# Kernel optimization log

Hardware: AMD Instinct MI355X
Metric: run time of the kernel (lower is better)

## Reference

```python
import jax, jax.numpy as jnp
import numpy as np

NUM_HEADS = 12  # head_dim = 768 // 12 = 64


def decomposed_rel_pos_bias(q, rel_pos_h, rel_pos_w, q_hw, k_hw):
    """Decomposed relative position bias (MViTv2 / SAM add_decomposed_rel_pos).
    q: (B*nH, q_h*q_w, head_dim). Returns bias (B*nH, q_h, q_w, k_h, k_w).
    q_size == k_size and rel_pos length == 2*size-1, so no interpolation branch.
    """
    q_h, q_w = q_hw
    k_h, k_w = k_hw
    # relative_coords = q_i - k_j + (k-1), values in [0, 2k-2]
    ch = jnp.arange(q_h)[:, None] - jnp.arange(k_h)[None, :] + (k_h - 1)
    cw = jnp.arange(q_w)[:, None] - jnp.arange(k_w)[None, :] + (k_w - 1)
    Rh = rel_pos_h[ch]  # (q_h, k_h, head_dim)
    Rw = rel_pos_w[cw]  # (q_w, k_w, head_dim)
    Bn, _, dim = q.shape
    r_q = q.reshape(Bn, q_h, q_w, dim)
    rel_h = jnp.einsum('bhwc,hkc->bhwk', r_q, Rh)  # (Bn, q_h, q_w, k_h)
    rel_w = jnp.einsum('bhwc,wkc->bhwk', r_q, Rw)  # (Bn, q_h, q_w, k_w)
    return rel_h[:, :, :, :, None] + rel_w[:, :, :, None, :]


def setup_inputs() -> dict:
    key = jax.random.key(0)
    ks = jax.random.split(key, 5)
    B, S, C = 200, 14, 768  # 200 windows of 14x14 tokens, dim 768
    hd = C // NUM_HEADS
    x = jax.random.normal(ks[0], (B, S, S, C), dtype=jnp.float32)
    w_qkv = jax.random.normal(ks[1], (C, 3 * C), dtype=jnp.float32) * (C ** -0.5)
    b_qkv = jnp.zeros((3 * C,), dtype=jnp.float32)
    w_proj = jax.random.normal(ks[2], (C, C), dtype=jnp.float32) * (C ** -0.5)
    b_proj = jnp.zeros((C,), dtype=jnp.float32)
    rel_pos_h = jax.random.normal(ks[3], (2 * S - 1, hd), dtype=jnp.float32) * 0.02
    rel_pos_w = jax.random.normal(ks[4], (2 * S - 1, hd), dtype=jnp.float32) * 0.02
    return {"x": x, "w_qkv": w_qkv, "b_qkv": b_qkv, "w_proj": w_proj,
            "b_proj": b_proj, "rel_pos_h": rel_pos_h, "rel_pos_w": rel_pos_w}


def reference(x, w_qkv, b_qkv, w_proj, b_proj, rel_pos_h, rel_pos_w):
    B, H, W, C = x.shape
    nH = NUM_HEADS
    hd = C // nH
    scale = hd ** -0.5
    # qkv projection: (B, H*W, 3*C)
    qkv = x.reshape(B, H * W, C) @ w_qkv + b_qkv
    qkv = qkv.reshape(B, H * W, 3, nH, hd).transpose(2, 0, 3, 1, 4)
    qkv = qkv.reshape(3, B * nH, H * W, hd)
    q, k, v = qkv[0], qkv[1], qkv[2]
    # attention scores with decomposed rel-pos bias
    attn = jnp.einsum('bqd,bkd->bqk', q * scale, k)  # (B*nH, HW, HW)
    bias = decomposed_rel_pos_bias(q, rel_pos_h, rel_pos_w, (H, W), (H, W))
    attn = attn.reshape(B * nH, H, W, H, W) + bias
    attn = jax.nn.softmax(attn.reshape(B * nH, H * W, H * W), axis=-1)
    out = jnp.einsum('bqk,bkd->bqd', attn, v)  # (B*nH, HW, hd)
    out = out.reshape(B, nH, H, W, hd).transpose(0, 2, 3, 1, 4).reshape(B, H, W, C)
    return out @ w_proj + b_proj
```

## Files before the change

kernel.cpp:

```cpp
#include <hip/hip_runtime.h>

typedef unsigned short u16;
typedef __attribute__((ext_vector_type(8))) __bf16 bf16x8;
typedef __attribute__((ext_vector_type(4))) float f32x4;
typedef __attribute__((ext_vector_type(4))) int i32x4;

#define MROWS 39200
#define MPAD  39296
#define KDIM  768

__device__ __forceinline__ u16 f2bf(float f) {
  unsigned u = __float_as_uint(f);
  return (u16)((u + 0x7fffu + ((u >> 16) & 1u)) >> 16);
}
__device__ __forceinline__ float bf2f(u16 b) {
  return __uint_as_float(((unsigned)b) << 16);
}
__device__ __forceinline__ f32x4 zero4() {
  f32x4 z; z[0] = 0.f; z[1] = 0.f; z[2] = 0.f; z[3] = 0.f; return z;
}
__device__ __forceinline__ void glds16(const void* g, void* l) {
  __builtin_amdgcn_global_load_lds((const __attribute__((address_space(1))) void*)(g),
                                   (__attribute__((address_space(3))) void*)(l), 16, 0, 0);
}

__global__ __launch_bounds__(256) void k_convert_x(const float* __restrict__ x,
                                                   u16* __restrict__ xb) {
  int idx = blockIdx.x * 256 + threadIdx.x;
  if (idx >= 3763200) return;
  f32x4 a = ((const f32x4*)x)[(size_t)idx * 2];
  f32x4 c = ((const f32x4*)x)[(size_t)idx * 2 + 1];
  u16 o[8];
  o[0] = f2bf(a[0]); o[1] = f2bf(a[1]); o[2] = f2bf(a[2]); o[3] = f2bf(a[3]);
  o[4] = f2bf(c[0]); o[5] = f2bf(c[1]); o[6] = f2bf(c[2]); o[7] = f2bf(c[3]);
  ((i32x4*)xb)[idx] = *(i32x4*)o;
}

__global__ __launch_bounds__(256) void k_transpose_w(const float* __restrict__ w,
                                                     u16* __restrict__ wT,
                                                     int K, int N, int total) {
  int idx = blockIdx.x * 256 + threadIdx.x;
  if (idx >= total) return;
  int n = idx / K, k = idx - n * K;
  wT[idx] = f2bf(w[(size_t)k * N + n]);
}

template <int MODE>
__global__ __launch_bounds__(256) void k_gemm(const u16* __restrict__ A,
                                              const u16* __restrict__ Bm,
                                              const float* __restrict__ bias,
                                              u16* __restrict__ o0,
                                              u16* __restrict__ o1,
                                              u16* __restrict__ o2,
                                              float* __restrict__ of) {
  __shared__ u16 a_sm[128 * 32];
  __shared__ u16 b_sm[128 * 32];
  const int tid = threadIdx.x, lane = tid & 63, wid = tid >> 6;
  const int tn = blockIdx.x, tm = blockIdx.y;
  const int lr = lane & 15, lg = lane >> 4;
  const int wm = wid >> 1, wn = wid & 1;

  const int o0b = wid * 2048 + lane * 16;
  const int o1b = o0b + 1024;
  const char* gA0 = (const char*)A + (size_t)(tm * 128 + (o0b >> 6)) * (KDIM * 2) + (o0b & 63);
  const char* gA1 = (const char*)A + (size_t)(tm * 128 + (o1b >> 6)) * (KDIM * 2) + (o1b & 63);
  const char* gB0 = (const char*)Bm + (size_t)(tn * 128 + (o0b >> 6)) * (KDIM * 2) + (o0b & 63);
  const char* gB1 = (const char*)Bm + (size_t)(tn * 128 + (o1b >> 6)) * (KDIM * 2) + (o1b & 63);
  char* lA0 = (char*)a_sm + wid * 2048;
  char* lA1 = lA0 + 1024;
  char* lB0 = (char*)b_sm + wid * 2048;
  char* lB1 = lB0 + 1024;

  f32x4 acc[4][4];
#pragma unroll
  for (int m = 0; m < 4; m++)
#pragma unroll
    for (int n = 0; n < 4; n++) acc[m][n] = zero4();

  for (int kt = 0; kt < KDIM / 32; kt++) {
    if (kt) __syncthreads();
    glds16(gA0 + kt * 64, lA0);
    glds16(gA1 + kt * 64, lA1);
    glds16(gB0 + kt * 64, lB0);
    glds16(gB1 + kt * 64, lB1);
    __syncthreads();
    bf16x8 af[4], bfr[4];
#pragma unroll
    for (int m = 0; m < 4; m++)
      af[m] = *(const bf16x8*)((const char*)a_sm + (wm * 64 + m * 16 + lr) * 64 + lg * 16);
#pragma unroll
    for (int n = 0; n < 4; n++)
      bfr[n] = *(const bf16x8*)((const char*)b_sm + (wn * 64 + n * 16 + lr) * 64 + lg * 16);
#pragma unroll
    for (int m = 0; m < 4; m++)
#pragma unroll
      for (int n = 0; n < 4; n++)
        acc[m][n] = __builtin_amdgcn_mfma_f32_16x16x32_bf16(af[m], bfr[n], acc[m][n], 0, 0, 0);
  }

#pragma unroll
  for (int n = 0; n < 4; n++) {
    int ng = tn * 128 + wn * 64 + n * 16 + lr;
    float bv = bias[ng];
#pragma unroll
    for (int m = 0; m < 4; m++) {
#pragma unroll
      for (int r = 0; r < 4; r++) {
        int mg = tm * 128 + wm * 64 + m * 16 + lg * 4 + r;
        if (mg < MROWS) {
          float val = acc[m][n][r] + bv;
          if (MODE == 0) {
            int which = ng / 768;
            int rem = ng - which * 768;
            int head = rem >> 6, d = rem & 63;
            int bi = mg / 196, i = mg - bi * 196;
            u16* dst = (which == 0) ? o0 : ((which == 1) ? o1 : o2);
            dst[((size_t)(bi * 12 + head) * 196 + i) * 64 + d] = f2bf(val);
          } else {
            of[(size_t)mg * 768 + ng] = val;
          }
        }
      }
    }
  }
}

#define SM_Q 0
#define SM_K 26624
#define SM_VT 53248
#define SM_P 81920
#define SM_RH 110592
#define SM_RW 122240
#define SM_TOTAL 133888

__global__ __launch_bounds__(256) void k_attn(const u16* __restrict__ qb,
                                              const u16* __restrict__ kb,
                                              const u16* __restrict__ vb,
                                              const float* __restrict__ rph,
                                              const float* __restrict__ rpw,
                                              u16* __restrict__ ao) {
  extern __shared__ char sm[];
  const int tid = threadIdx.x;
  const int bh = blockIdx.x;
  const size_t base = (size_t)bh * (196 * 64);

  for (int c = tid; c < 1568; c += 256) {
    int row = c >> 3, cb = (c & 7) << 4;
    int so = (row * 128 + cb) ^ ((row & 7) << 4);
    *(i32x4*)(sm + SM_Q + so) = *(const i32x4*)((const char*)(qb + base) + c * 16);
    *(i32x4*)(sm + SM_K + so) = *(const i32x4*)((const char*)(kb + base) + c * 16);
  }
  i32x4 zi; zi[0] = 0; zi[1] = 0; zi[2] = 0; zi[3] = 0;
  for (int c = tid; c < 96; c += 256) {
    int row = 196 + (c >> 3), cb = (c & 7) << 4;
    int so = (row * 128 + cb) ^ ((row & 7) << 4);
    *(i32x4*)(sm + SM_Q + so) = zi;
    *(i32x4*)(sm + SM_K + so) = zi;
  }
  for (int c = tid; c < 1568; c += 256) {
    int j = c >> 3, d0 = (c & 7) << 3;
    i32x4 vv = *(const i32x4*)((const char*)(vb + base) + c * 16);
    const u16* u = (const u16*)&vv;
#pragma unroll
    for (int e = 0; e < 8; e++) {
      int d = d0 + e;
      int so = (d * 448 + j * 2) ^ ((d & 7) << 4);
      *(u16*)(sm + SM_VT + so) = u[e];
    }
  }
  for (int idx = tid; idx < 64 * 28; idx += 256) {
    int d = idx / 28, j = 196 + (idx - d * 28);
    int so = (d * 448 + j * 2) ^ ((d & 7) << 4);
    *(u16*)(sm + SM_VT + so) = 0;
  }
  for (int idx = tid; idx < 1024; idx += 256) {
    int wv2 = idx >> 8, rem = idx & 255;
    int pr = rem >> 4, cc = 208 + (rem & 15);
    int so = wv2 * 7168 + ((pr * 448 + cc * 2) ^ ((pr & 7) << 4));
    *(u16*)(sm + SM_P + so) = 0;
  }
  __syncthreads();

  for (int e = tid; e < 208 * 14; e += 256) {
    int i = e / 14, kh = e - i * 14;
    float acc = 0.f;
    if (i < 196) {
      int h = i / 14;
      const float* R = rph + (h - kh + 13) * 64;
#pragma unroll
      for (int c8 = 0; c8 < 8; c8++) {
        int so = (i * 128 + c8 * 16) ^ ((i & 7) << 4);
        i32x4 v = *(const i32x4*)(sm + SM_Q + so);
        const u16* u = (const u16*)&v;
#pragma unroll
        for (int e2 = 0; e2 < 8; e2++) acc += bf2f(u[e2]) * R[c8 * 8 + e2];
      }
    }
    *(float*)(sm + SM_RH + e * 4) = acc;
  }
  for (int e = tid; e < 208 * 14; e += 256) {
    int i = e / 14, kw = e - i * 14;
    float acc = 0.f;
    if (i < 196) {
      int wq = i - (i / 14) * 14;
      const float* R = rpw + (wq - kw + 13) * 64;
#pragma unroll
      for (int c8 = 0; c8 < 8; c8++) {
        int so = (i * 128 + c8 * 16) ^ ((i & 7) << 4);
        i32x4 v = *(const i32x4*)(sm + SM_Q + so);
        const u16* u = (const u16*)&v;
#pragma unroll
        for (int e2 = 0; e2 < 8; e2++) acc += bf2f(u[e2]) * R[c8 * 8 + e2];
      }
    }
    *(float*)(sm + SM_RW + e * 4) = acc;
  }
  __syncthreads();

  const int lane = tid & 63, wv = tid >> 6;
  const int lr = lane & 15, lg = lane >> 4;
  const int bi = bh / 12, head = bh - bi * 12;

  for (int rt = wv; rt < 13; rt += 4) {
    int arow = rt * 16 + lr;
    bf16x8 aq0 = *(const bf16x8*)(sm + SM_Q + ((arow * 128 + lg * 16) ^ ((arow & 7) << 4)));
    bf16x8 aq1 = *(const bf16x8*)(sm + SM_Q + ((arow * 128 + 64 + lg * 16) ^ ((arow & 7) << 4)));
    f32x4 s[13];
#pragma unroll
    for (int j = 0; j < 13; j++) s[j] = zero4();
#pragma unroll
    for (int j = 0; j < 13; j++) {
      int brow = j * 16 + lr;
      bf16x8 bk0 = *(const bf16x8*)(sm + SM_K + ((brow * 128 + lg * 16) ^ ((brow & 7) << 4)));
      bf16x8 bk1 = *(const bf16x8*)(sm + SM_K + ((brow * 128 + 64 + lg * 16) ^ ((brow & 7) << 4)));
      s[j] = __builtin_amdgcn_mfma_f32_16x16x32_bf16(aq0, bk0, s[j], 0, 0, 0);
      s[j] = __builtin_amdgcn_mfma_f32_16x16x32_bf16(aq1, bk1, s[j], 0, 0, 0);
    }
    float rs[4];
#pragma unroll
    for (int r = 0; r < 4; r++) {
      int qi = rt * 16 + lg * 4 + r;
      float mx = -3.0e38f;
#pragma unroll
      for (int j = 0; j < 13; j++) {
        int col = j * 16 + lr;
        float t;
        if (col < 196) {
          int kh = (col * 2341) >> 15;
          int kw = col - kh * 14;
          t = s[j][r] * 0.125f + *(const float*)(sm + SM_RH + (qi * 14 + kh) * 4)
                               + *(const float*)(sm + SM_RW + (qi * 14 + kw) * 4);
        } else {
          t = -3.0e38f;
        }
        s[j][r] = t;
        mx = fmaxf(mx, t);
      }
      mx = fmaxf(mx, __shfl_xor(mx, 1));
      mx = fmaxf(mx, __shfl_xor(mx, 2));
      mx = fmaxf(mx, __shfl_xor(mx, 4));
      mx = fmaxf(mx, __shfl_xor(mx, 8));
      float sum = 0.f;
#pragma unroll
      for (int j = 0; j < 13; j++) {
        float p = __expf(s[j][r] - mx);
        s[j][r] = p;
        sum += p;
      }
      sum += __shfl_xor(sum, 1);
      sum += __shfl_xor(sum, 2);
      sum += __shfl_xor(sum, 4);
      sum += __shfl_xor(sum, 8);
      rs[r] = 1.f / sum;
    }
#pragma unroll
    for (int r = 0; r < 4; r++) {
      int pr = lg * 4 + r;
#pragma unroll
      for (int j = 0; j < 13; j++) {
        int col = j * 16 + lr;
        int so = wv * 7168 + ((pr * 448 + col * 2) ^ ((pr & 7) << 4));
        *(u16*)(sm + SM_P + so) = f2bf(s[j][r]);
      }
    }
    f32x4 ov[4];
#pragma unroll
    for (int d4 = 0; d4 < 4; d4++) ov[d4] = zero4();
#pragma unroll
    for (int kk = 0; kk < 7; kk++) {
      int soa = wv * 7168 + ((lr * 448 + kk * 64 + lg * 16) ^ ((lr & 7) << 4));
      bf16x8 pa = *(const bf16x8*)(sm + SM_P + soa);
#pragma unroll
      for (int d4 = 0; d4 < 4; d4++) {
        int vr = d4 * 16 + lr;
        int sob = (vr * 448 + kk * 64 + lg * 16) ^ ((vr & 7) << 4);
        bf16x8 vf = *(const bf16x8*)(sm + SM_VT + sob);
        ov[d4] = __builtin_amdgcn_mfma_f32_16x16x32_bf16(pa, vf, ov[d4], 0, 0, 0);
      }
    }
#pragma unroll
    for (int r = 0; r < 4; r++) {
      int i = rt * 16 + lg * 4 + r;
      if (i < 196) {
        size_t ro = ((size_t)(bi * 196 + i)) * 768 + head * 64;
#pragma unroll
        for (int d4 = 0; d4 < 4; d4++) {
          ao[ro + d4 * 16 + lr] = f2bf(ov[d4][r] * rs[r]);
        }
      }
    }
  }
}

extern "C" void kernel_launch(void* const* d_in, const int* in_sizes, int n_in,
                              void* d_out, int out_size, void* d_ws, size_t ws_size,
                              hipStream_t stream) {
  const float* x = (const float*)d_in[0];
  const float* w_qkv = (const float*)d_in[1];
  const float* b_qkv = (const float*)d_in[2];
  const float* w_proj = (const float*)d_in[3];
  const float* b_proj = (const float*)d_in[4];
  const float* rph = (const float*)d_in[5];
  const float* rpw = (const float*)d_in[6];
  float* out = (float*)d_out;

  char* ws = (char*)d_ws;
  u16* xb = (u16*)(ws + 0);
  u16* aob = (u16*)(ws + 0);
  u16* wqkvT = (u16*)(ws + 60358656);
  u16* wprojT = (u16*)(ws + 63897600);
  u16* qbuf = (u16*)(ws + 65077248);
  u16* kbuf = (u16*)(ws + 125288448);
  u16* vbuf = (u16*)(ws + 185499648);
  if (ws_size < 245710848ULL) return;

  k_convert_x<<<14700, 256, 0, stream>>>(x, xb);
  k_transpose_w<<<6912, 256, 0, stream>>>(w_qkv, wqkvT, 768, 2304, 768 * 2304);
  k_transpose_w<<<2304, 256, 0, stream>>>(w_proj, wprojT, 768, 768, 768 * 768);

  k_gemm<0><<<dim3(18, 307), 256, 0, stream>>>(xb, wqkvT, b_qkv, qbuf, kbuf, vbuf, nullptr);

  hipFuncSetAttribute((const void*)k_attn, hipFuncAttributeMaxDynamicSharedMemorySize, SM_TOTAL);
  k_attn<<<2400, 256, SM_TOTAL, stream>>>(qbuf, kbuf, vbuf, rph, rpw, aob);

  k_gemm<1><<<dim3(6, 307), 256, 0, stream>>>(aob, wprojT, b_proj, nullptr, nullptr, nullptr, out);
}
```

Baseline: 1.188 ms.

## Restructure attention kernel: MFMA rel-pos bias, register softmax, transposed V, XCD swizzle

Rewrites the attention kernel so the rel-pos bias projections run as MFMAs against a precomputed bf16 table instead of scalar loops. S is computed transposed so softmax reductions need only two cross-lane shuffles, and P is passed to the PV MFMA through register shuffles rather than an LDS round-trip. The QKV GEMM writes V pre-transposed, K is staged with global_load_lds, and LDS use drops to fit two blocks per CU. Both GEMMs gain an XCD-aware block remap for better L2 locality. Bias terms are now rounded to bf16, which adds some precision loss.

```diff
diff --git a/kernel.cpp b/kernel.cpp
--- a/kernel.cpp
+++ b/kernel.cpp
@@ -1,12 +1,13 @@
 #include <hip/hip_runtime.h>
 
 typedef unsigned short u16;
+typedef unsigned int u32;
 typedef __attribute__((ext_vector_type(8))) __bf16 bf16x8;
 typedef __attribute__((ext_vector_type(4))) float f32x4;
 typedef __attribute__((ext_vector_type(4))) int i32x4;
+typedef __attribute__((ext_vector_type(2))) int i32x2;
 
 #define MROWS 39200
-#define MPAD  39296
 #define KDIM  768
 
 __device__ __forceinline__ u16 f2bf(float f) {
@@ -22,6 +23,11 @@
 __device__ __forceinline__ void glds16(const void* g, void* l) {
   __builtin_amdgcn_global_load_lds((const __attribute__((address_space(1))) void*)(g),
                                    (__attribute__((address_space(3))) void*)(l), 16, 0, 0);
+}
+__device__ __forceinline__ u32 cvt_pk_bf16(float lo, float hi) {
+  u32 r;
+  asm volatile("v_cvt_pk_bf16_f32 %0, %1, %2" : "=v"(r) : "v"(lo), "v"(hi));
+  return r;
 }
 
 __global__ __launch_bounds__(256) void k_convert_x(const float* __restrict__ x,
@@ -45,6 +51,18 @@
   wT[idx] = f2bf(w[(size_t)k * N + n]);
 }
 
+__global__ __launch_bounds__(256) void k_prep_rpb(const float* __restrict__ rph,
+                                                  const float* __restrict__ rpw,
+                                                  u16* __restrict__ rpb) {
+  int idx = blockIdx.x * 256 + threadIdx.x;
+  if (idx >= 4096) return;
+  int p = idx >> 6, c = idx & 63;
+  float v = 0.f;
+  if (p < 27) v = rph[p * 64 + c];
+  else if (p >= 32 && p < 59) v = rpw[(p - 32) * 64 + c];
+  rpb[idx] = f2bf(v);
+}
+
 template <int MODE>
 __global__ __launch_bounds__(256) void k_gemm(const u16* __restrict__ A,
                                               const u16* __restrict__ Bm,
@@ -52,11 +70,15 @@
                                               u16* __restrict__ o0,
                                               u16* __restrict__ o1,
                                               u16* __restrict__ o2,
-                                              float* __restrict__ of) {
+                                              float* __restrict__ of,
+                                              int ntn, int swq, int swr) {
   __shared__ u16 a_sm[128 * 32];
   __shared__ u16 b_sm[128 * 32];
   const int tid = threadIdx.x, lane = tid & 63, wid = tid >> 6;
-  const int tn = blockIdx.x, tm = blockIdx.y;
+  int orig = blockIdx.x;
+  int xcd = orig & 7, jj = orig >> 3;
+  int wg = (xcd < swr ? xcd * (swq + 1) : swr * (swq + 1) + (xcd - swr) * swq) + jj;
+  const int tn = wg % ntn, tm = wg / ntn;
   const int lr = lane & 15, lg = lane >> 4;
   const int wm = wid >> 1, wn = wid & 1;
 
@@ -114,8 +136,13 @@
             int rem = ng - which * 768;
             int head = rem >> 6, d = rem & 63;
             int bi = mg / 196, i = mg - bi * 196;
-            u16* dst = (which == 0) ? o0 : ((which == 1) ? o1 : o2);
-            dst[((size_t)(bi * 12 + head) * 196 + i) * 64 + d] = f2bf(val);
+            int bh = bi * 12 + head;
+            if (which == 0)
+              o0[((size_t)bh * 196 + i) * 64 + d] = f2bf(val);
+            else if (which == 1)
+              o1[((size_t)bh * 196 + i) * 64 + d] = f2bf(val);
+            else
+              o2[((size_t)bh * 64 + d) * 196 + i] = f2bf(val);
           } else {
             of[(size_t)mg * 768 + ng] = val;
           }
@@ -125,187 +152,196 @@
   }
 }
 
-#define SM_Q 0
-#define SM_K 26624
-#define SM_VT 53248
-#define SM_P 81920
-#define SM_RH 110592
-#define SM_RW 122240
-#define SM_TOTAL 133888
-
-__global__ __launch_bounds__(256) void k_attn(const u16* __restrict__ qb,
-                                              const u16* __restrict__ kb,
-                                              const u16* __restrict__ vb,
-                                              const float* __restrict__ rph,
-                                              const float* __restrict__ rpw,
-                                              u16* __restrict__ ao) {
+#define AK 0
+#define AV 26624
+#define AT 55296
+#define SMT 78592
+
+__global__ __launch_bounds__(256, 2) void k_attn(const u16* __restrict__ qb,
+                                                 const u16* __restrict__ kb,
+                                                 const u16* __restrict__ vt,
+                                                 const u16* __restrict__ rpb,
+                                                 u16* __restrict__ ao) {
   extern __shared__ char sm[];
   const int tid = threadIdx.x;
   const int bh = blockIdx.x;
-  const size_t base = (size_t)bh * (196 * 64);
-
-  for (int c = tid; c < 1568; c += 256) {
-    int row = c >> 3, cb = (c & 7) << 4;
-    int so = (row * 128 + cb) ^ ((row & 7) << 4);
-    *(i32x4*)(sm + SM_Q + so) = *(const i32x4*)((const char*)(qb + base) + c * 16);
-    *(i32x4*)(sm + SM_K + so) = *(const i32x4*)((const char*)(kb + base) + c * 16);
-  }
-  i32x4 zi; zi[0] = 0; zi[1] = 0; zi[2] = 0; zi[3] = 0;
-  for (int c = tid; c < 96; c += 256) {
-    int row = 196 + (c >> 3), cb = (c & 7) << 4;
-    int so = (row * 128 + cb) ^ ((row & 7) << 4);
-    *(i32x4*)(sm + SM_Q + so) = zi;
-    *(i32x4*)(sm + SM_K + so) = zi;
-  }
-  for (int c = tid; c < 1568; c += 256) {
-    int j = c >> 3, d0 = (c & 7) << 3;
-    i32x4 vv = *(const i32x4*)((const char*)(vb + base) + c * 16);
-    const u16* u = (const u16*)&vv;
-#pragma unroll
-    for (int e = 0; e < 8; e++) {
-      int d = d0 + e;
-      int so = (d * 448 + j * 2) ^ ((d & 7) << 4);
-      *(u16*)(sm + SM_VT + so) = u[e];
-    }
-  }
-  for (int idx = tid; idx < 64 * 28; idx += 256) {
-    int d = idx / 28, j = 196 + (idx - d * 28);
-    int so = (d * 448 + j * 2) ^ ((d & 7) << 4);
-    *(u16*)(sm + SM_VT + so) = 0;
-  }
-  for (int idx = tid; idx < 1024; idx += 256) {
-    int wv2 = idx >> 8, rem = idx & 255;
-    int pr = rem >> 4, cc = 208 + (rem & 15);
-    int so = wv2 * 7168 + ((pr * 448 + cc * 2) ^ ((pr & 7) << 4));
-    *(u16*)(sm + SM_P + so) = 0;
-  }
-  __syncthreads();
-
-  for (int e = tid; e < 208 * 14; e += 256) {
-    int i = e / 14, kh = e - i * 14;
-    float acc = 0.f;
-    if (i < 196) {
-      int h = i / 14;
-      const float* R = rph + (h - kh + 13) * 64;
-#pragma unroll
-      for (int c8 = 0; c8 < 8; c8++) {
-        int so = (i * 128 + c8 * 16) ^ ((i & 7) << 4);
-        i32x4 v = *(const i32x4*)(sm + SM_Q + so);
-        const u16* u = (const u16*)&v;
-#pragma unroll
-        for (int e2 = 0; e2 < 8; e2++) acc += bf2f(u[e2]) * R[c8 * 8 + e2];
-      }
-    }
-    *(float*)(sm + SM_RH + e * 4) = acc;
-  }
-  for (int e = tid; e < 208 * 14; e += 256) {
-    int i = e / 14, kw = e - i * 14;
-    float acc = 0.f;
-    if (i < 196) {
-      int wq = i - (i / 14) * 14;
-      const float* R = rpw + (wq - kw + 13) * 64;
-#pragma unroll
-      for (int c8 = 0; c8 < 8; c8++) {
-        int so = (i * 128 + c8 * 16) ^ ((i & 7) << 4);
-        i32x4 v = *(const i32x4*)(sm + SM_Q + so);
-        const u16* u = (const u16*)&v;
-#pragma unroll
-        for (int e2 = 0; e2 < 8; e2++) acc += bf2f(u[e2]) * R[c8 * 8 + e2];
-      }
-    }
-    *(float*)(sm + SM_RW + e * 4) = acc;
-  }
-  __syncthreads();
-
   const int lane = tid & 63, wv = tid >> 6;
   const int lr = lane & 15, lg = lane >> 4;
+  const u16* qg = qb + (size_t)bh * 12544;
+  const u16* kg = kb + (size_t)bh * 12544;
+  const u16* vg = vt + (size_t)bh * 12544;
+
+  for (int o = tid * 16; o < 25088; o += 4096) {
+    int row = o >> 7, cb = o & 127;
+    glds16((const char*)kg + row * 128 + (cb ^ ((row & 7) << 4)), sm + AK + o);
+  }
+  for (int ch = tid; ch < 1600; ch += 256) {
+    int d = ch / 25, i = ch - d * 25;
+    const char* src = (const char*)vg + d * 392 + i * 16;
+    int dst = (d * 448 + i * 16) ^ ((d & 7) << 4);
+    if (i < 24) {
+      i32x2 va = *(const i32x2*)src;
+      i32x2 vb = *(const i32x2*)(src + 8);
+      *(i32x2*)(sm + AV + dst) = va;
+      *(i32x2*)(sm + AV + dst + 8) = vb;
+    } else {
+      i32x2 va = *(const i32x2*)src;
+      *(i32x2*)(sm + AV + dst) = va;
+    }
+  }
+  {
+    int d = tid >> 2, part = tid & 3;
+    if (part == 0) {
+      i32x2 z; z[0] = 0; z[1] = 0;
+      *(i32x2*)(sm + AV + ((d * 448 + 392) ^ ((d & 7) << 4))) = z;
+    } else {
+      i32x4 z; z[0] = 0; z[1] = 0; z[2] = 0; z[3] = 0;
+      *(i32x4*)(sm + AV + ((d * 448 + 384 + part * 16) ^ ((d & 7) << 4))) = z;
+    }
+  }
+  __syncthreads();
+
+  bf16x8 rb0[4], rb1[4];
+#pragma unroll
+  for (int pt = 0; pt < 4; pt++) {
+    rb0[pt] = *(const bf16x8*)((const char*)rpb + (pt * 16 + lr) * 128 + lg * 16);
+    rb1[pt] = *(const bf16x8*)((const char*)rpb + (pt * 16 + lr) * 128 + 64 + lg * 16);
+  }
+
   const int bi = bh / 12, head = bh - bi * 12;
 
-  for (int rt = wv; rt < 13; rt += 4) {
-    int arow = rt * 16 + lr;
-    bf16x8 aq0 = *(const bf16x8*)(sm + SM_Q + ((arow * 128 + lg * 16) ^ ((arow & 7) << 4)));
-    bf16x8 aq1 = *(const bf16x8*)(sm + SM_Q + ((arow * 128 + 64 + lg * 16) ^ ((arow & 7) << 4)));
+  for (int qt = wv; qt < 13; qt += 4) {
+    const int q = qt * 16 + lr;
+    const int qc = q > 195 ? 195 : q;
+    bf16x8 bq0 = *(const bf16x8*)((const char*)qg + qc * 128 + lg * 16);
+    bf16x8 bq1 = *(const bf16x8*)((const char*)qg + qc * 128 + 64 + lg * 16);
+
+    {
+      f32x4 td[4];
+#pragma unroll
+      for (int pt = 0; pt < 4; pt++) {
+        td[pt] = zero4();
+        td[pt] = __builtin_amdgcn_mfma_f32_16x16x32_bf16(bq0, rb0[pt], td[pt], 0, 0, 0);
+        td[pt] = __builtin_amdgcn_mfma_f32_16x16x32_bf16(bq1, rb1[pt], td[pt], 0, 0, 0);
+      }
+#pragma unroll
+      for (int pt = 0; pt < 4; pt++) {
+        int p = pt * 16 + lr;
+        int col = (p < 28) ? p : ((p >= 32 && p < 60) ? p - 4 : -1);
+        if (col >= 0) {
+#pragma unroll
+          for (int r = 0; r < 4; r++) {
+            int rowq = qt * 16 + lg * 4 + r;
+            *(u16*)(sm + AT + rowq * 112 + col * 2) = f2bf(td[pt][r]);
+          }
+        }
+      }
+      asm volatile("s_waitcnt lgkmcnt(0)" ::: "memory");
+    }
+
     f32x4 s[13];
 #pragma unroll
     for (int j = 0; j < 13; j++) s[j] = zero4();
 #pragma unroll
     for (int j = 0; j < 13; j++) {
-      int brow = j * 16 + lr;
-      bf16x8 bk0 = *(const bf16x8*)(sm + SM_K + ((brow * 128 + lg * 16) ^ ((brow & 7) << 4)));
-      bf16x8 bk1 = *(const bf16x8*)(sm + SM_K + ((brow * 128 + 64 + lg * 16) ^ ((brow & 7) << 4)));
-      s[j] = __builtin_amdgcn_mfma_f32_16x16x32_bf16(aq0, bk0, s[j], 0, 0, 0);
-      s[j] = __builtin_amdgcn_mfma_f32_16x16x32_bf16(aq1, bk1, s[j], 0, 0, 0);
-    }
-    float rs[4];
-#pragma unroll
-    for (int r = 0; r < 4; r++) {
-      int qi = rt * 16 + lg * 4 + r;
-      float mx = -3.0e38f;
-#pragma unroll
-      for (int j = 0; j < 13; j++) {
-        int col = j * 16 + lr;
-        float t;
-        if (col < 196) {
-          int kh = (col * 2341) >> 15;
-          int kw = col - kh * 14;
-          t = s[j][r] * 0.125f + *(const float*)(sm + SM_RH + (qi * 14 + kh) * 4)
-                               + *(const float*)(sm + SM_RW + (qi * 14 + kw) * 4);
-        } else {
-          t = -3.0e38f;
+      int kr = j * 16 + lr;
+      bf16x8 ak0 = *(const bf16x8*)(sm + AK + ((kr * 128 + lg * 16) ^ ((kr & 7) << 4)));
+      bf16x8 ak1 = *(const bf16x8*)(sm + AK + ((kr * 128 + 64 + lg * 16) ^ ((kr & 7) << 4)));
+      s[j] = __builtin_amdgcn_mfma_f32_16x16x32_bf16(ak0, bq0, s[j], 0, 0, 0);
+      s[j] = __builtin_amdgcn_mfma_f32_16x16x32_bf16(ak1, bq1, s[j], 0, 0, 0);
+    }
+
+    const int hq = (q * 2341) >> 15;
+    const int wq = q - hq * 14;
+    const char* Trow = sm + AT + q * 112;
+    float mx = -3.0e38f;
+#pragma unroll
+    for (int j = 0; j < 13; j++) {
+#pragma unroll
+      for (int r = 0; r < 4; r++) {
+        int k = j * 16 + lg * 4 + r;
+        float t = -3.0e38f;
+        if (k < 196) {
+          int kh = (k * 2341) >> 15;
+          int kw = k - kh * 14;
+          t = s[j][r] * 0.125f
+            + bf2f(*(const u16*)(Trow + (hq - kh + 13) * 2))
+            + bf2f(*(const u16*)(Trow + (wq - kw + 13 + 28) * 2));
         }
         s[j][r] = t;
         mx = fmaxf(mx, t);
       }
-      mx = fmaxf(mx, __shfl_xor(mx, 1));
-      mx = fmaxf(mx, __shfl_xor(mx, 2));
-      mx = fmaxf(mx, __shfl_xor(mx, 4));
-      mx = fmaxf(mx, __shfl_xor(mx, 8));
-      float sum = 0.f;
-#pragma unroll
-      for (int j = 0; j < 13; j++) {
-        float p = __expf(s[j][r] - mx);
+    }
+    mx = fmaxf(mx, __shfl_xor(mx, 16));
+    mx = fmaxf(mx, __shfl_xor(mx, 32));
+    float sum = 0.f;
+#pragma unroll
+    for (int j = 0; j < 13; j++) {
+#pragma unroll
+      for (int r = 0; r < 4; r++) {
+        int k = j * 16 + lg * 4 + r;
+        float p = 0.f;
+        if (k < 196) p = __expf(s[j][r] - mx);
         s[j][r] = p;
         sum += p;
       }
-      sum += __shfl_xor(sum, 1);
-      sum += __shfl_xor(sum, 2);
-      sum += __shfl_xor(sum, 4);
-      sum += __shfl_xor(sum, 8);
-      rs[r] = 1.f / sum;
-    }
-#pragma unroll
-    for (int r = 0; r < 4; r++) {
-      int pr = lg * 4 + r;
-#pragma unroll
-      for (int j = 0; j < 13; j++) {
-        int col = j * 16 + lr;
-        int so = wv * 7168 + ((pr * 448 + col * 2) ^ ((pr & 7) << 4));
-        *(u16*)(sm + SM_P + so) = f2bf(s[j][r]);
-      }
-    }
+    }
+    sum += __shfl_xor(sum, 16);
+    sum += __shfl_xor(sum, 32);
+    const float rs = 1.f / sum;
+
+    u32 w[13][2];
+#pragma unroll
+    for (int j = 0; j < 13; j++) {
+      w[j][0] = cvt_pk_bf16(s[j][0] * rs, s[j][1] * rs);
+      w[j][1] = cvt_pk_bf16(s[j][2] * rs, s[j][3] * rs);
+    }
+
+    const int srcA = lr + ((lg & 1) * 2) * 16;
+    const int srcB = srcA + 16;
+    const bool hi = (lg >> 1) != 0;
+
     f32x4 ov[4];
 #pragma unroll
     for (int d4 = 0; d4 < 4; d4++) ov[d4] = zero4();
+
 #pragma unroll
     for (int kk = 0; kk < 7; kk++) {
-      int soa = wv * 7168 + ((lr * 448 + kk * 64 + lg * 16) ^ ((lr & 7) << 4));
-      bf16x8 pa = *(const bf16x8*)(sm + SM_P + soa);
+      u32 W[4];
+      if (kk < 6) {
+#pragma unroll
+        for (int m = 0; m < 4; m++) {
+          int src = (m < 2) ? srcA : srcB;
+          u32 ta = (u32)__shfl((int)w[2 * kk][m & 1], src);
+          u32 tb = (u32)__shfl((int)w[2 * kk + 1][m & 1], src);
+          W[m] = hi ? tb : ta;
+        }
+      } else {
+#pragma unroll
+        for (int m = 0; m < 4; m++) {
+          int src = (m < 2) ? srcA : srcB;
+          u32 ta = (u32)__shfl((int)w[12][m & 1], src);
+          W[m] = hi ? 0u : ta;
+        }
+      }
+      i32x4 wi; wi[0] = W[0]; wi[1] = W[1]; wi[2] = W[2]; wi[3] = W[3];
+      bf16x8 pa = *(bf16x8*)&wi;
 #pragma unroll
       for (int d4 = 0; d4 < 4; d4++) {
         int vr = d4 * 16 + lr;
-        int sob = (vr * 448 + kk * 64 + lg * 16) ^ ((vr & 7) << 4);
-        bf16x8 vf = *(const bf16x8*)(sm + SM_VT + sob);
+        bf16x8 vf = *(const bf16x8*)(sm + AV + ((vr * 448 + kk * 64 + lg * 16) ^ ((vr & 7) << 4)));
         ov[d4] = __builtin_amdgcn_mfma_f32_16x16x32_bf16(pa, vf, ov[d4], 0, 0, 0);
       }
     }
+
 #pragma unroll
     for (int r = 0; r < 4; r++) {
-      int i = rt * 16 + lg * 4 + r;
+      int i = qt * 16 + lg * 4 + r;
       if (i < 196) {
-        size_t ro = ((size_t)(bi * 196 + i)) * 768 + head * 64;
+        size_t ro = ((size_t)(bi * 196 + i)) * 768 + head * 64 + lr;
 #pragma unroll
         for (int d4 = 0; d4 < 4; d4++) {
-          ao[ro + d4 * 16 + lr] = f2bf(ov[d4][r] * rs[r]);
+          ao[ro + d4 * 16] = f2bf(ov[d4][r]);
         }
       }
     }
@@ -327,21 +363,25 @@
   char* ws = (char*)d_ws;
   u16* xb = (u16*)(ws + 0);
   u16* aob = (u16*)(ws + 0);
+  u16* rpb = (u16*)(ws + 60211200);
   u16* wqkvT = (u16*)(ws + 60358656);
   u16* wprojT = (u16*)(ws + 63897600);
   u16* qbuf = (u16*)(ws + 65077248);
   u16* kbuf = (u16*)(ws + 125288448);
-  u16* vbuf = (u16*)(ws + 185499648);
+  u16* vtg = (u16*)(ws + 185499648);
   if (ws_size < 245710848ULL) return;
 
+  k_prep_rpb<<<16, 256, 0, stream>>>(rph, rpw, rpb);
   k_convert_x<<<14700, 256, 0, stream>>>(x, xb);
   k_transpose_w<<<6912, 256, 0, stream>>>(w_qkv, wqkvT, 768, 2304, 768 * 2304);
   k_transpose_w<<<2304, 256, 0, stream>>>(w_proj, wprojT, 768, 768, 768 * 768);
 
-  k_gemm<0><<<dim3(18, 307), 256, 0, stream>>>(xb, wqkvT, b_qkv, qbuf, kbuf, vbuf, nullptr);
-
-  hipFuncSetAttribute((const void*)k_attn, hipFuncAttributeMaxDynamicSharedMemorySize, SM_TOTAL);
-  k_attn<<<2400, 256, SM_TOTAL, stream>>>(qbuf, kbuf, vbuf, rph, rpw, aob);
-
-  k_gemm<1><<<dim3(6, 307), 256, 0, stream>>>(aob, wprojT, b_proj, nullptr, nullptr, nullptr, out);
-}
+  k_gemm<0><<<5526, 256, 0, stream>>>(xb, wqkvT, b_qkv, qbuf, kbuf, vtg, nullptr,
+                                      18, 690, 6);
+
+  hipFuncSetAttribute((const void*)k_attn, hipFuncAttributeMaxDynamicSharedMemorySize, SMT);
+  k_attn<<<2400, 256, SMT, stream>>>(qbuf, kbuf, vtg, rpb, aob);
+
+  k_gemm<1><<<1842, 256, 0, stream>>>(aob, wprojT, b_proj, nullptr, nullptr, nullptr, out,
+                                      6, 230, 2);
+}
```

New measurement: 988.7 us. 16.8% less time.
